# Kernel optimization log

Measured on AMD Instinct MI355X. Metric: run time of the kernel, lower is better.

Reference implementation:

```python
import jax, jax.numpy as jnp
import numpy as np

B, S, P, L, H = 64, 512, 32, 30, 768
FH = 1024  # fc_hidden_size


def setup_inputs() -> dict:
    key = jax.random.key(0)
    ks = jax.random.split(key, 8)
    token_embeddings = jax.random.normal(ks[0], (B, S, H), jnp.float32)
    pooler_output = jax.random.normal(ks[1], (B, H), jnp.float32)
    num_positions = jax.random.randint(ks[2], (B, P), 0, S)
    # labels: 0/1 codes, with trailing slots per example padded with -1 rows
    lab = jax.random.randint(ks[3], (B, P, L), 0, 2).astype(jnp.float32)
    valid = jax.random.randint(ks[4], (B, 1), 8, P + 1)  # num real slots per example
    row = jnp.arange(P)[None, :]
    lab = jnp.where((row < valid)[:, :, None], lab, -1.0)
    num_codes_labels = lab.reshape(B, P * L)
    W1 = jax.random.normal(ks[5], (2 * H, FH), jnp.float32) / np.sqrt(2 * H)
    b1 = jnp.zeros((FH,), jnp.float32)
    W2 = jax.random.normal(ks[6], (FH, FH // 2), jnp.float32) / np.sqrt(FH)
    b2 = jnp.zeros((FH // 2,), jnp.float32)
    W3 = jax.random.normal(ks[7], (FH // 2, L), jnp.float32) / np.sqrt(FH // 2)
    b3 = jnp.zeros((L,), jnp.float32)
    return {"token_embeddings": token_embeddings, "pooler_output": pooler_output,
            "num_positions": num_positions, "num_codes_labels": num_codes_labels,
            "W1": W1, "b1": b1, "W2": W2, "b2": b2, "W3": W3, "b3": b3}


def reference(token_embeddings, pooler_output, num_positions, num_codes_labels,
              W1, b1, W2, b2, W3, b3):
    # gather number-token hidden states: [B, P, H]
    p_hidden = jnp.take_along_axis(token_embeddings, num_positions[:, :, None], axis=1)
    feat = jnp.concatenate(
        [p_hidden, jnp.broadcast_to(pooler_output[:, None, :], p_hidden.shape)], axis=-1)
    # Batch_Net_CLS head. NOTE: original uses nn.LeakyReLU(True) -> negative_slope=1.0,
    # which is mathematically the identity, so the activations are omitted (faithful).
    h = feat @ W1 + b1
    h = h @ W2 + b2
    logits = h @ W3 + b3  # [B, P, L]

    labels = num_codes_labels.reshape(B, -1, L)
    pad_pre = jnp.any(labels != -1.0, axis=-1)  # [B, P] True for real slots
    mf = pad_pre.astype(jnp.float32)

    # BCEWithLogitsLoss over non-pad elements: softplus(x) - x*y, mean
    bce_elem = jax.nn.softplus(logits) - logits * labels
    bce_loss = jnp.sum(bce_elem * mf[:, :, None]) / (jnp.sum(mf) * L)

    binary = (jax.nn.sigmoid(logits) > 0.5).astype(jnp.float32)
    count_out = jnp.sum(binary, axis=-1)
    count_lab = jnp.sum(labels, axis=-1)
    count_loss = jnp.mean((count_out - count_lab) ** 2 * mf)

    # position loss: only slots where both counts are exactly 1 (single-hot)
    eq = (count_out == 1.0) & (count_lab == 1.0)
    pos_out = jnp.argmax(binary, axis=-1).astype(jnp.float32)
    pos_lab = jnp.argmax(labels, axis=-1).astype(jnp.float32)
    n_eq = jnp.sum(eq.astype(jnp.float32))
    pos_sum = jnp.sum((pos_out - pos_lab) ** 2 * eq.astype(jnp.float32))
    position_loss = jnp.where(n_eq > 0, pos_sum / jnp.maximum(n_eq, 1.0), 0.0)

    return bce_loss + 10.0 * count_loss + 5.0 * position_loss
```

## Files before the change

kernel.cpp:

```cpp
#include <hip/hip_runtime.h>
#include <cstddef>
#include <cstdint>

#define Mq   2048
#define Lq   30
#define N1q  1024
#define N2q  512
#define K1q  1536
#define Hq   768
#define NBLK 512
#define Z1   2
#define Z2   4

typedef float    f32x4 __attribute__((ext_vector_type(4)));
typedef _Float16 f16x8 __attribute__((ext_vector_type(8)));

#define GLD16(gptr, lptr) \
  __builtin_amdgcn_global_load_lds((const __attribute__((address_space(1))) void*)(gptr), \
                                   (__attribute__((address_space(3))) void*)(lptr), 16, 0, 0)

__device__ void transpose_tile(const float* __restrict__ src,
                               _Float16* __restrict__ dst,
                               int K, int N, int k0, int n0) {
  __shared__ float T[64][65];
  const int t = threadIdx.x;
  {
    const int kl = t >> 2, nc = (t & 3) * 16;
    const float* s = src + (size_t)(k0 + kl) * N + n0 + nc;
    float4 v0 = *(const float4*)s;
    float4 v1 = *(const float4*)(s + 4);
    float4 v2 = *(const float4*)(s + 8);
    float4 v3 = *(const float4*)(s + 12);
    T[nc + 0][kl] = v0.x; T[nc + 1][kl] = v0.y; T[nc + 2][kl] = v0.z; T[nc + 3][kl] = v0.w;
    T[nc + 4][kl] = v1.x; T[nc + 5][kl] = v1.y; T[nc + 6][kl] = v1.z; T[nc + 7][kl] = v1.w;
    T[nc + 8][kl] = v2.x; T[nc + 9][kl] = v2.y; T[nc +10][kl] = v2.z; T[nc +11][kl] = v2.w;
    T[nc +12][kl] = v3.x; T[nc +13][kl] = v3.y; T[nc +14][kl] = v3.z; T[nc +15][kl] = v3.w;
  }
  __syncthreads();
  {
    const int nl = t >> 2, kc = (t & 3) * 16;
    __align__(16) _Float16 tmp[16];
    #pragma unroll
    for (int i = 0; i < 16; ++i) tmp[i] = (_Float16)T[nl][kc + i];
    _Float16* d = dst + (size_t)(n0 + nl) * K + k0 + kc;
    *(uint4*)d       = *(const uint4*)tmp;
    *(uint4*)(d + 8) = *(const uint4*)(tmp + 8);
  }
}

__global__ __launch_bounds__(256)
void prep_all(const float* __restrict__ tok, const float* __restrict__ pool,
              const int* __restrict__ npos, const float* __restrict__ W1,
              const float* __restrict__ W2, _Float16* __restrict__ A1,
              _Float16* __restrict__ W1T, _Float16* __restrict__ W2T) {
  const int bid = blockIdx.x, tid = threadIdx.x;
  if (bid < 256) {
    const int q = tid >> 5, l32 = tid & 31;
    const int m = bid * 8 + q;
    const int bI = m >> 5, p = m & 31;
    const int pos = npos[bI * 32 + p];
    const float* src1 = tok + ((size_t)bI * 512 + pos) * Hq;
    const float* src2 = pool + (size_t)bI * Hq;
    _Float16* dst = A1 + (size_t)m * K1q;
    for (int g = l32; g < 384; g += 32) {
      const float* s = (g < 192) ? (src1 + g * 4) : (src2 + (g - 192) * 4);
      float4 v = *(const float4*)s;
      __align__(8) _Float16 o[4] = {(_Float16)v.x, (_Float16)v.y, (_Float16)v.z, (_Float16)v.w};
      *(uint2*)(dst + g * 4) = *(const uint2*)o;
    }
  } else if (bid < 640) {
    const int idx = bid - 256;
    transpose_tile(W1, W1T, K1q, N1q, (idx / 16) * 64, (idx % 16) * 64);
  } else {
    const int idx = bid - 640;
    transpose_tile(W2, W2T, N1q, N2q, (idx / 8) * 64, (idx % 8) * 64);
  }
}

__global__ __launch_bounds__(256)
void gemm1_f16(const _Float16* __restrict__ A, const _Float16* __restrict__ BT,
               _Float16* __restrict__ Cpart) {
  __shared__ _Float16 As[128 * 32];
  __shared__ _Float16 Bs[128 * 32];
  const int tid = threadIdx.x, w = tid >> 6, lane = tid & 63;
  const int n0 = blockIdx.x * 128, m0 = blockIdx.y * 128, z = blockIdx.z;
  const int ml = lane & 15, g4 = lane >> 4;
  const int wm = (w >> 1) * 64, wn = (w & 1) * 64;

  f32x4 acc[4][4];
  #pragma unroll
  for (int i = 0; i < 4; ++i)
    #pragma unroll
    for (int j = 0; j < 4; ++j)
      #pragma unroll
      for (int r = 0; r < 4; ++r) acc[i][j][r] = 0.f;

  const int rs0 = w * 32 + (lane >> 2);
  const int cl  = lane & 3;

  for (int it = 0; it < (K1q / Z1) / 32; ++it) {
    const int kt = z * (K1q / Z1) + it * 32;
    __syncthreads();
    #pragma unroll
    for (int t = 0; t < 2; ++t) {
      const int r  = rs0 + t * 16;
      const int cs = cl ^ ((r >> 1) & 3);
      GLD16(A  + (size_t)(m0 + r) * K1q + kt + cs * 8, As + (w * 32 + t * 16) * 32);
      GLD16(BT + (size_t)(n0 + r) * K1q + kt + cs * 8, Bs + (w * 32 + t * 16) * 32);
    }
    __syncthreads();
    f16x8 af[4], bf[4];
    #pragma unroll
    for (int i = 0; i < 4; ++i) {
      const int ar = wm + i * 16 + ml;
      af[i] = *(const f16x8*)(As + ar * 32 + ((g4 ^ ((ar >> 1) & 3)) << 3));
      const int br = wn + i * 16 + ml;
      bf[i] = *(const f16x8*)(Bs + br * 32 + ((g4 ^ ((br >> 1) & 3)) << 3));
    }
    #pragma unroll
    for (int i = 0; i < 4; ++i)
      #pragma unroll
      for (int j = 0; j < 4; ++j)
        acc[i][j] = __builtin_amdgcn_mfma_f32_16x16x32_f16(bf[j], af[i], acc[i][j], 0, 0, 0);
  }

  _Float16* Cp = Cpart + (size_t)z * Mq * N1q;
  #pragma unroll
  for (int i = 0; i < 4; ++i) {
    const int row = m0 + wm + i * 16 + ml;
    #pragma unroll
    for (int j = 0; j < 4; ++j) {
      const int col = n0 + wn + j * 16 + g4 * 4;
      __align__(8) _Float16 o[4] = {(_Float16)acc[i][j][0], (_Float16)acc[i][j][1],
                                    (_Float16)acc[i][j][2], (_Float16)acc[i][j][3]};
      *(uint2*)(Cp + (size_t)row * N1q + col) = *(const uint2*)o;
    }
  }
}

__global__ __launch_bounds__(256)
void gemm2_fused(const _Float16* __restrict__ C1, const float* __restrict__ b1,
                 const _Float16* __restrict__ BT, float* __restrict__ Cpart) {
  __shared__ _Float16 As[128 * 32];
  __shared__ _Float16 Bs[128 * 32];
  const int tid = threadIdx.x, w = tid >> 6, lane = tid & 63;
  const int n0 = blockIdx.x * 128, m0 = blockIdx.y * 128, z = blockIdx.z;
  const int ml = lane & 15, g4 = lane >> 4;
  const int wm = (w >> 1) * 64, wn = (w & 1) * 64;
  const size_t MN1 = (size_t)Mq * N1q;

  f32x4 acc[4][4];
  #pragma unroll
  for (int i = 0; i < 4; ++i)
    #pragma unroll
    for (int j = 0; j < 4; ++j)
      #pragma unroll
      for (int r = 0; r < 4; ++r) acc[i][j][r] = 0.f;

  const int rs0 = w * 32 + (lane >> 2);
  const int cl  = lane & 3;
  const int r2  = tid >> 1, half = tid & 1;

  for (int it = 0; it < (N1q / Z2) / 32; ++it) {
    const int kt = z * (N1q / Z2) + it * 32;
    __syncthreads();
    #pragma unroll
    for (int t = 0; t < 2; ++t) {
      const int r  = rs0 + t * 16;
      const int cs = cl ^ ((r >> 1) & 3);
      GLD16(BT + (size_t)(n0 + r) * N1q + kt + cs * 8, Bs + (w * 32 + t * 16) * 32);
    }
    {
      const _Float16* p = C1 + (size_t)(m0 + r2) * N1q + kt + half * 16;
      f16x8 u0 = *(const f16x8*)p;
      f16x8 u1 = *(const f16x8*)(p + 8);
      f16x8 v0 = *(const f16x8*)(p + MN1);
      f16x8 v1 = *(const f16x8*)(p + MN1 + 8);
      const float* bb = b1 + kt + half * 16;
      f16x8 o0, o1;
      #pragma unroll
      for (int e = 0; e < 8; ++e) {
        o0[e] = (_Float16)((float)u0[e] + (float)v0[e] + bb[e]);
        o1[e] = (_Float16)((float)u1[e] + (float)v1[e] + bb[e + 8]);
      }
      const int s  = (r2 >> 1) & 3;
      *(f16x8*)(As + r2 * 32 + (((half * 2)     ^ s) << 3)) = o0;
      *(f16x8*)(As + r2 * 32 + (((half * 2 + 1) ^ s) << 3)) = o1;
    }
    __syncthreads();
    f16x8 af[4], bf[4];
    #pragma unroll
    for (int i = 0; i < 4; ++i) {
      const int ar = wm + i * 16 + ml;
      af[i] = *(const f16x8*)(As + ar * 32 + ((g4 ^ ((ar >> 1) & 3)) << 3));
      const int br = wn + i * 16 + ml;
      bf[i] = *(const f16x8*)(Bs + br * 32 + ((g4 ^ ((br >> 1) & 3)) << 3));
    }
    #pragma unroll
    for (int i = 0; i < 4; ++i)
      #pragma unroll
      for (int j = 0; j < 4; ++j)
        acc[i][j] = __builtin_amdgcn_mfma_f32_16x16x32_f16(bf[j], af[i], acc[i][j], 0, 0, 0);
  }

  float* Cp = Cpart + (size_t)z * Mq * N2q;
  #pragma unroll
  for (int i = 0; i < 4; ++i) {
    const int row = m0 + wm + i * 16 + ml;
    #pragma unroll
    for (int j = 0; j < 4; ++j) {
      const int col = n0 + wn + j * 16 + g4 * 4;
      *(float4*)(Cp + (size_t)row * N2q + col) = *(const float4*)&acc[i][j];
    }
  }
}

__global__ __launch_bounds__(256)
void loss_kernel(const float* __restrict__ C2, const float* __restrict__ b2,
                 const float* __restrict__ W3, const float* __restrict__ b3,
                 const float* __restrict__ labels, float* __restrict__ part) {
  __shared__ float hrow[4][512];
  __shared__ float red[4][5];
  const int tid = threadIdx.x, w = tid >> 6, lane = tid & 63;
  const int m = blockIdx.x * 4 + w;
  const size_t MN2 = (size_t)Mq * N2q;

  {
    const int k = lane * 8;
    float4 s0 = *(const float4*)(b2 + k);
    float4 s1 = *(const float4*)(b2 + k + 4);
    const float* cp = C2 + (size_t)m * N2q + k;
    #pragma unroll
    for (int z = 0; z < Z2; ++z) {
      float4 v0 = *(const float4*)(cp + (size_t)z * MN2);
      float4 v1 = *(const float4*)(cp + (size_t)z * MN2 + 4);
      s0.x += v0.x; s0.y += v0.y; s0.z += v0.z; s0.w += v0.w;
      s1.x += v1.x; s1.y += v1.y; s1.z += v1.z; s1.w += v1.w;
    }
    *(float4*)&hrow[w][k]     = s0;
    *(float4*)&hrow[w][k + 4] = s1;
  }
  __syncthreads();

  const int c  = lane & 31;
  const int kh = lane >> 5;
  float a0 = 0.f, a1 = 0.f, a2 = 0.f, a3 = 0.f;
  if (c < Lq) {
    const float* hp = hrow[w] + kh * 256;
    const float* wp = W3 + (size_t)(kh * 256) * Lq + c;
    #pragma unroll 4
    for (int i = 0; i < 256; i += 4) {
      a0 = fmaf(hp[i],     wp[(i)     * Lq], a0);
      a1 = fmaf(hp[i + 1], wp[(i + 1) * Lq], a1);
      a2 = fmaf(hp[i + 2], wp[(i + 2) * Lq], a2);
      a3 = fmaf(hp[i + 3], wp[(i + 3) * Lq], a3);
    }
  }
  float a = (a0 + a1) + (a2 + a3);
  a += __shfl_xor(a, 32);

  const bool act = lane < Lq;
  float logit = 0.f, lab = 0.f;
  if (act) {
    logit = a + b3[lane];
    lab = labels[(size_t)m * Lq + lane];
  }

  const unsigned long long validmask = __ballot(act && lab != -1.0f);
  const unsigned long long outmask   = __ballot(act && logit > 0.0f);
  const unsigned long long labmask   = __ballot(act && lab == 1.0f);
  const bool valid = (validmask != 0ULL);
  const int count_out = __popcll(outmask);
  const int count_lab = __popcll(labmask);

  float bce = 0.f;
  if (act && valid) {
    const float x = logit;
    bce = fmaxf(x, 0.f) + log1pf(expf(-fabsf(x))) - x * lab;
  }
  bce += __shfl_xor(bce, 16); bce += __shfl_xor(bce, 8);
  bce += __shfl_xor(bce, 4);  bce += __shfl_xor(bce, 2);
  bce += __shfl_xor(bce, 1);

  if (lane == 0) {
    float pb = 0.f, pv = 0.f, pc = 0.f, pe = 0.f, pp = 0.f;
    if (valid) {
      pb = bce; pv = 1.f;
      const float d = (float)count_out - (float)count_lab;
      pc = d * d;
    }
    if (count_out == 1 && count_lab == 1) {
      const float po = (float)(__ffsll((long long)outmask) - 1);
      const float pl = (float)(__ffsll((long long)labmask) - 1);
      pe = 1.f;
      const float dp = po - pl;
      pp = dp * dp;
    }
    red[w][0] = pb; red[w][1] = pv; red[w][2] = pc; red[w][3] = pe; red[w][4] = pp;
  }
  __syncthreads();
  if (tid < 5) {
    part[blockIdx.x * 5 + tid] =
        red[0][tid] + red[1][tid] + red[2][tid] + red[3][tid];
  }
}

__global__ __launch_bounds__(256)
void finalize_kernel(const float* __restrict__ part, float* __restrict__ out) {
  __shared__ float red[32][5];
  const int t = threadIdx.x;
  if (t < 160) {
    const int j = t % 5, grp = t / 5;
    float s = 0.f;
    for (int i = grp; i < NBLK; i += 32) s += part[i * 5 + j];
    red[grp][j] = s;
  }
  __syncthreads();
  if (t == 0) {
    float t0 = 0.f, t1 = 0.f, t2 = 0.f, t3 = 0.f, t4 = 0.f;
    #pragma unroll
    for (int g = 0; g < 32; ++g) {
      t0 += red[g][0]; t1 += red[g][1]; t2 += red[g][2];
      t3 += red[g][3]; t4 += red[g][4];
    }
    const float bce = t0 / (t1 * (float)Lq);
    const float cnt = 10.0f * t2 / (float)Mq;
    const float pos = (t3 > 0.f) ? 5.0f * t4 / fmaxf(t3, 1.0f) : 0.f;
    out[0] = bce + cnt + pos;
  }
}

extern "C" void kernel_launch(void* const* d_in, const int* in_sizes, int n_in,
                              void* d_out, int out_size, void* d_ws, size_t ws_size,
                              hipStream_t stream) {
  const float* tok    = (const float*)d_in[0];
  const float* pool   = (const float*)d_in[1];
  const int*   npos   = (const int*)  d_in[2];
  const float* labels = (const float*)d_in[3];
  const float* W1     = (const float*)d_in[4];
  const float* b1     = (const float*)d_in[5];
  const float* W2     = (const float*)d_in[6];
  const float* b2     = (const float*)d_in[7];
  const float* W3     = (const float*)d_in[8];
  const float* b3     = (const float*)d_in[9];
  float* out = (float*)d_out;

  char* ws = (char*)d_ws;
  _Float16* A1   = (_Float16*)(ws + 0x00000000);
  _Float16* C1p  = (_Float16*)(ws + 0x00600000);
  _Float16* W1T  = (_Float16*)(ws + 0x00E00000);
  _Float16* W2T  = (_Float16*)(ws + 0x01100000);
  float*    C2p  = (float*)   (ws + 0x01200000);
  float*    part = (float*)   (ws + 0x02200000);

  prep_all<<<768, 256, 0, stream>>>(tok, pool, npos, W1, W2, A1, W1T, W2T);
  gemm1_f16<<<dim3(8, 16, Z1), 256, 0, stream>>>(A1, W1T, C1p);
  gemm2_fused<<<dim3(4, 16, Z2), 256, 0, stream>>>(C1p, b1, W2T, C2p);
  loss_kernel<<<NBLK, 256, 0, stream>>>(C2p, b2, W3, b3, labels, part);
  finalize_kernel<<<1, 256, 0, stream>>>(part, out);
}
```

Before: 203.5 us.

## Fuse all stages into one cooperative persistent kernel with double-buffered GEMMs

Replaces the five separate launches with a single cooperative kernel of 256 blocks that uses grid.sync between the prep, GEMM1, GEMM2, loss and finalize stages. Both GEMM main loops now double-buffer their LDS tiles so the next tile's loads overlap the current MFMAs. The b1 bias is folded algebraically into a precomputed b2' = b2 + b1·W2, which removes the per-element bias add from GEMM2. The aim is to cut launch gaps and load latency. In exchange, grid-wide barriers are added and only 256 blocks run, below the 512 and 768 blocks some stages used before.

```diff
diff --git a/kernel.cpp b/kernel.cpp
--- a/kernel.cpp
+++ b/kernel.cpp
@@ -1,6 +1,9 @@
 #include <hip/hip_runtime.h>
+#include <hip/hip_cooperative_groups.h>
 #include <cstddef>
 #include <cstdint>
+
+namespace cg = cooperative_groups;
 
 #define Mq   2048
 #define Lq   30
@@ -21,8 +24,8 @@
 
 __device__ void transpose_tile(const float* __restrict__ src,
                                _Float16* __restrict__ dst,
-                               int K, int N, int k0, int n0) {
-  __shared__ float T[64][65];
+                               int K, int N, int k0, int n0,
+                               float (*T)[65]) {
   const int t = threadIdx.x;
   {
     const int kl = t >> 2, nc = (t & 3) * 16;
@@ -46,287 +49,335 @@
     *(uint4*)d       = *(const uint4*)tmp;
     *(uint4*)(d + 8) = *(const uint4*)(tmp + 8);
   }
+  __syncthreads();
 }
 
 __global__ __launch_bounds__(256)
-void prep_all(const float* __restrict__ tok, const float* __restrict__ pool,
-              const int* __restrict__ npos, const float* __restrict__ W1,
-              const float* __restrict__ W2, _Float16* __restrict__ A1,
-              _Float16* __restrict__ W1T, _Float16* __restrict__ W2T) {
+void mega(const float* __restrict__ tok, const float* __restrict__ pool,
+          const int* __restrict__ npos, const float* __restrict__ labels,
+          const float* __restrict__ W1, const float* __restrict__ b1,
+          const float* __restrict__ W2, const float* __restrict__ b2,
+          const float* __restrict__ W3, const float* __restrict__ b3,
+          char* __restrict__ ws, float* __restrict__ out)
+{
+  __shared__ __align__(16) unsigned char SMEM[32768];
+
+  _Float16* A1   = (_Float16*)(ws + 0x00000000);
+  _Float16* C1p  = (_Float16*)(ws + 0x00600000);
+  _Float16* W1T  = (_Float16*)(ws + 0x00E00000);
+  _Float16* W2T  = (_Float16*)(ws + 0x01100000);
+  float*    C2p  = (float*)   (ws + 0x01200000);
+  float*    part = (float*)   (ws + 0x02200000);
+  float*    b2p  = (float*)   (ws + 0x02210000);
+
   const int bid = blockIdx.x, tid = threadIdx.x;
-  if (bid < 256) {
-    const int q = tid >> 5, l32 = tid & 31;
-    const int m = bid * 8 + q;
-    const int bI = m >> 5, p = m & 31;
-    const int pos = npos[bI * 32 + p];
-    const float* src1 = tok + ((size_t)bI * 512 + pos) * Hq;
-    const float* src2 = pool + (size_t)bI * Hq;
-    _Float16* dst = A1 + (size_t)m * K1q;
-    for (int g = l32; g < 384; g += 32) {
-      const float* s = (g < 192) ? (src1 + g * 4) : (src2 + (g - 192) * 4);
-      float4 v = *(const float4*)s;
-      __align__(8) _Float16 o[4] = {(_Float16)v.x, (_Float16)v.y, (_Float16)v.z, (_Float16)v.w};
-      *(uint2*)(dst + g * 4) = *(const uint2*)o;
-    }
-  } else if (bid < 640) {
-    const int idx = bid - 256;
-    transpose_tile(W1, W1T, K1q, N1q, (idx / 16) * 64, (idx % 16) * 64);
-  } else {
-    const int idx = bid - 640;
-    transpose_tile(W2, W2T, N1q, N2q, (idx / 8) * 64, (idx % 8) * 64);
-  }
-}
-
-__global__ __launch_bounds__(256)
-void gemm1_f16(const _Float16* __restrict__ A, const _Float16* __restrict__ BT,
-               _Float16* __restrict__ Cpart) {
-  __shared__ _Float16 As[128 * 32];
-  __shared__ _Float16 Bs[128 * 32];
-  const int tid = threadIdx.x, w = tid >> 6, lane = tid & 63;
-  const int n0 = blockIdx.x * 128, m0 = blockIdx.y * 128, z = blockIdx.z;
-  const int ml = lane & 15, g4 = lane >> 4;
-  const int wm = (w >> 1) * 64, wn = (w & 1) * 64;
-
-  f32x4 acc[4][4];
-  #pragma unroll
-  for (int i = 0; i < 4; ++i)
+  const int w = tid >> 6, lane = tid & 63;
+  cg::grid_group grid = cg::this_grid();
+
+  {
+    float (*T)[65] = (float(*)[65])SMEM;
+    #pragma unroll 1
+    for (int i = 0; i < 3; ++i) {
+      const int u = bid + 256 * i;
+      if (u < 256) {
+        const int q = tid >> 5, l32 = tid & 31;
+        const int m = u * 8 + q;
+        const int bI = m >> 5, p = m & 31;
+        const int pos = npos[bI * 32 + p];
+        const float* src1 = tok + ((size_t)bI * 512 + pos) * Hq;
+        const float* src2 = pool + (size_t)bI * Hq;
+        _Float16* dst = A1 + (size_t)m * K1q;
+        for (int g = l32; g < 384; g += 32) {
+          const float* s = (g < 192) ? (src1 + g * 4) : (src2 + (g - 192) * 4);
+          float4 v = *(const float4*)s;
+          __align__(8) _Float16 o[4] = {(_Float16)v.x, (_Float16)v.y, (_Float16)v.z, (_Float16)v.w};
+          *(uint2*)(dst + g * 4) = *(const uint2*)o;
+        }
+      } else if (u < 640) {
+        const int idx = u - 256;
+        transpose_tile(W1, W1T, K1q, N1q, (idx / 16) * 64, (idx % 16) * 64, T);
+      } else {
+        const int idx = u - 640;
+        transpose_tile(W2, W2T, N1q, N2q, (idx / 8) * 64, (idx % 8) * 64, T);
+      }
+    }
+    if (bid < 8) {
+      const int c  = bid * 64 + (tid >> 2);
+      const int ks = (tid & 3) * 256;
+      float s = 0.f;
+      for (int k = 0; k < 256; ++k)
+        s = fmaf(b1[ks + k], W2[(size_t)(ks + k) * N2q + c], s);
+      s += __shfl_xor(s, 1);
+      s += __shfl_xor(s, 2);
+      if ((tid & 3) == 0) b2p[c] = b2[c] + s;
+    }
+  }
+  grid.sync();
+
+  {
+    _Float16* As = (_Float16*)SMEM;
+    _Float16* Bs = (_Float16*)(SMEM + 16384);
+    const int bx = bid & 7, by = (bid >> 3) & 15, z = bid >> 7;
+    const int n0 = bx * 128, m0 = by * 128;
+    const int ml = lane & 15, g4 = lane >> 4;
+    const int wm = (w >> 1) * 64, wn = (w & 1) * 64;
+    const int rs0 = w * 32 + (lane >> 2);
+    const int cl  = lane & 3;
+    const int kbase = z * (K1q / Z1);
+
+    f32x4 acc[4][4];
     #pragma unroll
-    for (int j = 0; j < 4; ++j)
-      #pragma unroll
-      for (int r = 0; r < 4; ++r) acc[i][j][r] = 0.f;
-
-  const int rs0 = w * 32 + (lane >> 2);
-  const int cl  = lane & 3;
-
-  for (int it = 0; it < (K1q / Z1) / 32; ++it) {
-    const int kt = z * (K1q / Z1) + it * 32;
+    for (int i = 0; i < 4; ++i)
+      #pragma unroll
+      for (int j = 0; j < 4; ++j)
+        #pragma unroll
+        for (int r = 0; r < 4; ++r) acc[i][j][r] = 0.f;
+
+    auto stage1 = [&](int it, int b) {
+      const int kt = kbase + it * 32;
+      #pragma unroll
+      for (int t = 0; t < 2; ++t) {
+        const int r  = rs0 + t * 16;
+        const int cs = cl ^ ((r >> 1) & 3);
+        GLD16(A1  + (size_t)(m0 + r) * K1q + kt + cs * 8, As + b * 4096 + (w * 32 + t * 16) * 32);
+        GLD16(W1T + (size_t)(n0 + r) * K1q + kt + cs * 8, Bs + b * 4096 + (w * 32 + t * 16) * 32);
+      }
+    };
+
+    stage1(0, 0);
     __syncthreads();
-    #pragma unroll
-    for (int t = 0; t < 2; ++t) {
-      const int r  = rs0 + t * 16;
-      const int cs = cl ^ ((r >> 1) & 3);
-      GLD16(A  + (size_t)(m0 + r) * K1q + kt + cs * 8, As + (w * 32 + t * 16) * 32);
-      GLD16(BT + (size_t)(n0 + r) * K1q + kt + cs * 8, Bs + (w * 32 + t * 16) * 32);
-    }
-    __syncthreads();
-    f16x8 af[4], bf[4];
+    int cur = 0;
+    #pragma unroll 1
+    for (int it = 0; it < (K1q / Z1) / 32; ++it) {
+      if (it < (K1q / Z1) / 32 - 1) stage1(it + 1, cur ^ 1);
+      f16x8 af[4], bf[4];
+      #pragma unroll
+      for (int i = 0; i < 4; ++i) {
+        const int ar = wm + i * 16 + ml;
+        af[i] = *(const f16x8*)(As + cur * 4096 + ar * 32 + ((g4 ^ ((ar >> 1) & 3)) << 3));
+        const int br = wn + i * 16 + ml;
+        bf[i] = *(const f16x8*)(Bs + cur * 4096 + br * 32 + ((g4 ^ ((br >> 1) & 3)) << 3));
+      }
+      #pragma unroll
+      for (int i = 0; i < 4; ++i)
+        #pragma unroll
+        for (int j = 0; j < 4; ++j)
+          acc[i][j] = __builtin_amdgcn_mfma_f32_16x16x32_f16(bf[j], af[i], acc[i][j], 0, 0, 0);
+      __syncthreads();
+      cur ^= 1;
+    }
+
+    _Float16* Cp = C1p + (size_t)z * Mq * N1q;
     #pragma unroll
     for (int i = 0; i < 4; ++i) {
-      const int ar = wm + i * 16 + ml;
-      af[i] = *(const f16x8*)(As + ar * 32 + ((g4 ^ ((ar >> 1) & 3)) << 3));
-      const int br = wn + i * 16 + ml;
-      bf[i] = *(const f16x8*)(Bs + br * 32 + ((g4 ^ ((br >> 1) & 3)) << 3));
-    }
+      const int row = m0 + wm + i * 16 + ml;
+      #pragma unroll
+      for (int j = 0; j < 4; ++j) {
+        const int col = n0 + wn + j * 16 + g4 * 4;
+        __align__(8) _Float16 o[4] = {(_Float16)acc[i][j][0], (_Float16)acc[i][j][1],
+                                      (_Float16)acc[i][j][2], (_Float16)acc[i][j][3]};
+        *(uint2*)(Cp + (size_t)row * N1q + col) = *(const uint2*)o;
+      }
+    }
+  }
+  grid.sync();
+
+  {
+    _Float16* As = (_Float16*)SMEM;
+    _Float16* Bs = (_Float16*)(SMEM + 16384);
+    const int bx = bid & 3, by = (bid >> 2) & 15, z = bid >> 6;
+    const int n0 = bx * 128, m0 = by * 128;
+    const int ml = lane & 15, g4 = lane >> 4;
+    const int wm = (w >> 1) * 64, wn = (w & 1) * 64;
+    const int rs0 = w * 32 + (lane >> 2);
+    const int cl  = lane & 3;
+    const int r2  = tid >> 1, half = tid & 1;
+    const size_t MN1 = (size_t)Mq * N1q;
+    const int kb2 = z * (N1q / Z2);
+
+    f32x4 acc[4][4];
     #pragma unroll
     for (int i = 0; i < 4; ++i)
       #pragma unroll
       for (int j = 0; j < 4; ++j)
-        acc[i][j] = __builtin_amdgcn_mfma_f32_16x16x32_f16(bf[j], af[i], acc[i][j], 0, 0, 0);
-  }
-
-  _Float16* Cp = Cpart + (size_t)z * Mq * N1q;
-  #pragma unroll
-  for (int i = 0; i < 4; ++i) {
-    const int row = m0 + wm + i * 16 + ml;
-    #pragma unroll
-    for (int j = 0; j < 4; ++j) {
-      const int col = n0 + wn + j * 16 + g4 * 4;
-      __align__(8) _Float16 o[4] = {(_Float16)acc[i][j][0], (_Float16)acc[i][j][1],
-                                    (_Float16)acc[i][j][2], (_Float16)acc[i][j][3]};
-      *(uint2*)(Cp + (size_t)row * N1q + col) = *(const uint2*)o;
-    }
-  }
-}
-
-__global__ __launch_bounds__(256)
-void gemm2_fused(const _Float16* __restrict__ C1, const float* __restrict__ b1,
-                 const _Float16* __restrict__ BT, float* __restrict__ Cpart) {
-  __shared__ _Float16 As[128 * 32];
-  __shared__ _Float16 Bs[128 * 32];
-  const int tid = threadIdx.x, w = tid >> 6, lane = tid & 63;
-  const int n0 = blockIdx.x * 128, m0 = blockIdx.y * 128, z = blockIdx.z;
-  const int ml = lane & 15, g4 = lane >> 4;
-  const int wm = (w >> 1) * 64, wn = (w & 1) * 64;
-  const size_t MN1 = (size_t)Mq * N1q;
-
-  f32x4 acc[4][4];
-  #pragma unroll
-  for (int i = 0; i < 4; ++i)
-    #pragma unroll
-    for (int j = 0; j < 4; ++j)
-      #pragma unroll
-      for (int r = 0; r < 4; ++r) acc[i][j][r] = 0.f;
-
-  const int rs0 = w * 32 + (lane >> 2);
-  const int cl  = lane & 3;
-  const int r2  = tid >> 1, half = tid & 1;
-
-  for (int it = 0; it < (N1q / Z2) / 32; ++it) {
-    const int kt = z * (N1q / Z2) + it * 32;
+        #pragma unroll
+        for (int r = 0; r < 4; ++r) acc[i][j][r] = 0.f;
+
+    f16x8 u0, u1, v0, v1;
+    auto issueA2 = [&](int it) {
+      const _Float16* p = C1p + (size_t)(m0 + r2) * N1q + kb2 + it * 32 + half * 16;
+      u0 = *(const f16x8*)p;         u1 = *(const f16x8*)(p + 8);
+      v0 = *(const f16x8*)(p + MN1); v1 = *(const f16x8*)(p + MN1 + 8);
+    };
+    auto stageB2 = [&](int it, int b) {
+      const int kt = kb2 + it * 32;
+      #pragma unroll
+      for (int t = 0; t < 2; ++t) {
+        const int r  = rs0 + t * 16;
+        const int cs = cl ^ ((r >> 1) & 3);
+        GLD16(W2T + (size_t)(n0 + r) * N1q + kt + cs * 8, Bs + b * 4096 + (w * 32 + t * 16) * 32);
+      }
+    };
+    auto writeA2 = [&](int b) {
+      f16x8 o0, o1;
+      #pragma unroll
+      for (int e = 0; e < 8; ++e) {
+        o0[e] = (_Float16)((float)u0[e] + (float)v0[e]);
+        o1[e] = (_Float16)((float)u1[e] + (float)v1[e]);
+      }
+      const int s = (r2 >> 1) & 3;
+      *(f16x8*)(As + b * 4096 + r2 * 32 + (((half * 2)     ^ s) << 3)) = o0;
+      *(f16x8*)(As + b * 4096 + r2 * 32 + (((half * 2 + 1) ^ s) << 3)) = o1;
+    };
+
+    issueA2(0); stageB2(0, 0); writeA2(0);
     __syncthreads();
-    #pragma unroll
-    for (int t = 0; t < 2; ++t) {
-      const int r  = rs0 + t * 16;
-      const int cs = cl ^ ((r >> 1) & 3);
-      GLD16(BT + (size_t)(n0 + r) * N1q + kt + cs * 8, Bs + (w * 32 + t * 16) * 32);
-    }
-    {
-      const _Float16* p = C1 + (size_t)(m0 + r2) * N1q + kt + half * 16;
-      f16x8 u0 = *(const f16x8*)p;
-      f16x8 u1 = *(const f16x8*)(p + 8);
-      f16x8 v0 = *(const f16x8*)(p + MN1);
-      f16x8 v1 = *(const f16x8*)(p + MN1 + 8);
-      const float* bb = b1 + kt + half * 16;
-      f16x8 o0, o1;
-      #pragma unroll
-      for (int e = 0; e < 8; ++e) {
-        o0[e] = (_Float16)((float)u0[e] + (float)v0[e] + bb[e]);
-        o1[e] = (_Float16)((float)u1[e] + (float)v1[e] + bb[e + 8]);
-      }
-      const int s  = (r2 >> 1) & 3;
-      *(f16x8*)(As + r2 * 32 + (((half * 2)     ^ s) << 3)) = o0;
-      *(f16x8*)(As + r2 * 32 + (((half * 2 + 1) ^ s) << 3)) = o1;
-    }
-    __syncthreads();
-    f16x8 af[4], bf[4];
+    int cur = 0;
+    #pragma unroll 1
+    for (int it = 0; it < (N1q / Z2) / 32; ++it) {
+      if (it < (N1q / Z2) / 32 - 1) { issueA2(it + 1); stageB2(it + 1, cur ^ 1); }
+      f16x8 af[4], bf[4];
+      #pragma unroll
+      for (int i = 0; i < 4; ++i) {
+        const int ar = wm + i * 16 + ml;
+        af[i] = *(const f16x8*)(As + cur * 4096 + ar * 32 + ((g4 ^ ((ar >> 1) & 3)) << 3));
+        const int br = wn + i * 16 + ml;
+        bf[i] = *(const f16x8*)(Bs + cur * 4096 + br * 32 + ((g4 ^ ((br >> 1) & 3)) << 3));
+      }
+      #pragma unroll
+      for (int i = 0; i < 4; ++i)
+        #pragma unroll
+        for (int j = 0; j < 4; ++j)
+          acc[i][j] = __builtin_amdgcn_mfma_f32_16x16x32_f16(bf[j], af[i], acc[i][j], 0, 0, 0);
+      if (it < (N1q / Z2) / 32 - 1) writeA2(cur ^ 1);
+      __syncthreads();
+      cur ^= 1;
+    }
+
+    float* Cp = C2p + (size_t)z * Mq * N2q;
     #pragma unroll
     for (int i = 0; i < 4; ++i) {
-      const int ar = wm + i * 16 + ml;
-      af[i] = *(const f16x8*)(As + ar * 32 + ((g4 ^ ((ar >> 1) & 3)) << 3));
-      const int br = wn + i * 16 + ml;
-      bf[i] = *(const f16x8*)(Bs + br * 32 + ((g4 ^ ((br >> 1) & 3)) << 3));
-    }
-    #pragma unroll
-    for (int i = 0; i < 4; ++i)
-      #pragma unroll
-      for (int j = 0; j < 4; ++j)
-        acc[i][j] = __builtin_amdgcn_mfma_f32_16x16x32_f16(bf[j], af[i], acc[i][j], 0, 0, 0);
-  }
-
-  float* Cp = Cpart + (size_t)z * Mq * N2q;
-  #pragma unroll
-  for (int i = 0; i < 4; ++i) {
-    const int row = m0 + wm + i * 16 + ml;
-    #pragma unroll
-    for (int j = 0; j < 4; ++j) {
-      const int col = n0 + wn + j * 16 + g4 * 4;
-      *(float4*)(Cp + (size_t)row * N2q + col) = *(const float4*)&acc[i][j];
-    }
-  }
-}
-
-__global__ __launch_bounds__(256)
-void loss_kernel(const float* __restrict__ C2, const float* __restrict__ b2,
-                 const float* __restrict__ W3, const float* __restrict__ b3,
-                 const float* __restrict__ labels, float* __restrict__ part) {
-  __shared__ float hrow[4][512];
-  __shared__ float red[4][5];
-  const int tid = threadIdx.x, w = tid >> 6, lane = tid & 63;
-  const int m = blockIdx.x * 4 + w;
-  const size_t MN2 = (size_t)Mq * N2q;
-
-  {
-    const int k = lane * 8;
-    float4 s0 = *(const float4*)(b2 + k);
-    float4 s1 = *(const float4*)(b2 + k + 4);
-    const float* cp = C2 + (size_t)m * N2q + k;
-    #pragma unroll
-    for (int z = 0; z < Z2; ++z) {
-      float4 v0 = *(const float4*)(cp + (size_t)z * MN2);
-      float4 v1 = *(const float4*)(cp + (size_t)z * MN2 + 4);
-      s0.x += v0.x; s0.y += v0.y; s0.z += v0.z; s0.w += v0.w;
-      s1.x += v1.x; s1.y += v1.y; s1.z += v1.z; s1.w += v1.w;
-    }
-    *(float4*)&hrow[w][k]     = s0;
-    *(float4*)&hrow[w][k + 4] = s1;
-  }
-  __syncthreads();
-
-  const int c  = lane & 31;
-  const int kh = lane >> 5;
-  float a0 = 0.f, a1 = 0.f, a2 = 0.f, a3 = 0.f;
-  if (c < Lq) {
-    const float* hp = hrow[w] + kh * 256;
-    const float* wp = W3 + (size_t)(kh * 256) * Lq + c;
-    #pragma unroll 4
-    for (int i = 0; i < 256; i += 4) {
-      a0 = fmaf(hp[i],     wp[(i)     * Lq], a0);
-      a1 = fmaf(hp[i + 1], wp[(i + 1) * Lq], a1);
-      a2 = fmaf(hp[i + 2], wp[(i + 2) * Lq], a2);
-      a3 = fmaf(hp[i + 3], wp[(i + 3) * Lq], a3);
-    }
-  }
-  float a = (a0 + a1) + (a2 + a3);
-  a += __shfl_xor(a, 32);
-
-  const bool act = lane < Lq;
-  float logit = 0.f, lab = 0.f;
-  if (act) {
-    logit = a + b3[lane];
-    lab = labels[(size_t)m * Lq + lane];
-  }
-
-  const unsigned long long validmask = __ballot(act && lab != -1.0f);
-  const unsigned long long outmask   = __ballot(act && logit > 0.0f);
-  const unsigned long long labmask   = __ballot(act && lab == 1.0f);
-  const bool valid = (validmask != 0ULL);
-  const int count_out = __popcll(outmask);
-  const int count_lab = __popcll(labmask);
-
-  float bce = 0.f;
-  if (act && valid) {
-    const float x = logit;
-    bce = fmaxf(x, 0.f) + log1pf(expf(-fabsf(x))) - x * lab;
-  }
-  bce += __shfl_xor(bce, 16); bce += __shfl_xor(bce, 8);
-  bce += __shfl_xor(bce, 4);  bce += __shfl_xor(bce, 2);
-  bce += __shfl_xor(bce, 1);
-
-  if (lane == 0) {
-    float pb = 0.f, pv = 0.f, pc = 0.f, pe = 0.f, pp = 0.f;
-    if (valid) {
-      pb = bce; pv = 1.f;
-      const float d = (float)count_out - (float)count_lab;
-      pc = d * d;
-    }
-    if (count_out == 1 && count_lab == 1) {
-      const float po = (float)(__ffsll((long long)outmask) - 1);
-      const float pl = (float)(__ffsll((long long)labmask) - 1);
-      pe = 1.f;
-      const float dp = po - pl;
-      pp = dp * dp;
-    }
-    red[w][0] = pb; red[w][1] = pv; red[w][2] = pc; red[w][3] = pe; red[w][4] = pp;
-  }
-  __syncthreads();
-  if (tid < 5) {
-    part[blockIdx.x * 5 + tid] =
-        red[0][tid] + red[1][tid] + red[2][tid] + red[3][tid];
-  }
-}
-
-__global__ __launch_bounds__(256)
-void finalize_kernel(const float* __restrict__ part, float* __restrict__ out) {
-  __shared__ float red[32][5];
-  const int t = threadIdx.x;
-  if (t < 160) {
-    const int j = t % 5, grp = t / 5;
-    float s = 0.f;
-    for (int i = grp; i < NBLK; i += 32) s += part[i * 5 + j];
-    red[grp][j] = s;
-  }
-  __syncthreads();
-  if (t == 0) {
-    float t0 = 0.f, t1 = 0.f, t2 = 0.f, t3 = 0.f, t4 = 0.f;
-    #pragma unroll
-    for (int g = 0; g < 32; ++g) {
-      t0 += red[g][0]; t1 += red[g][1]; t2 += red[g][2];
-      t3 += red[g][3]; t4 += red[g][4];
-    }
-    const float bce = t0 / (t1 * (float)Lq);
-    const float cnt = 10.0f * t2 / (float)Mq;
-    const float pos = (t3 > 0.f) ? 5.0f * t4 / fmaxf(t3, 1.0f) : 0.f;
-    out[0] = bce + cnt + pos;
+      const int row = m0 + wm + i * 16 + ml;
+      #pragma unroll
+      for (int j = 0; j < 4; ++j) {
+        const int col = n0 + wn + j * 16 + g4 * 4;
+        *(float4*)(Cp + (size_t)row * N2q + col) = *(const float4*)&acc[i][j];
+      }
+    }
+  }
+  grid.sync();
+
+  {
+    float (*hrow)[512] = (float(*)[512])SMEM;
+    float (*red)[5]    = (float(*)[5])(SMEM + 8192);
+    const size_t MN2 = (size_t)Mq * N2q;
+    #pragma unroll 1
+    for (int i = 0; i < 2; ++i) {
+      const int u = bid * 2 + i;
+      const int m = u * 4 + w;
+      __syncthreads();
+      {
+        const int k = lane * 8;
+        float4 s0 = *(const float4*)(b2p + k);
+        float4 s1 = *(const float4*)(b2p + k + 4);
+        const float* cp = C2p + (size_t)m * N2q + k;
+        #pragma unroll
+        for (int zz = 0; zz < Z2; ++zz) {
+          float4 q0 = *(const float4*)(cp + (size_t)zz * MN2);
+          float4 q1 = *(const float4*)(cp + (size_t)zz * MN2 + 4);
+          s0.x += q0.x; s0.y += q0.y; s0.z += q0.z; s0.w += q0.w;
+          s1.x += q1.x; s1.y += q1.y; s1.z += q1.z; s1.w += q1.w;
+        }
+        *(float4*)&hrow[w][k]     = s0;
+        *(float4*)&hrow[w][k + 4] = s1;
+      }
+      __syncthreads();
+
+      const int c  = lane & 31;
+      const int kh = lane >> 5;
+      float a0 = 0.f, a1 = 0.f, a2 = 0.f, a3 = 0.f;
+      if (c < Lq) {
+        const float* hp = hrow[w] + kh * 256;
+        const float* wp = W3 + (size_t)(kh * 256) * Lq + c;
+        #pragma unroll 4
+        for (int k = 0; k < 256; k += 4) {
+          a0 = fmaf(hp[k],     wp[(k)     * Lq], a0);
+          a1 = fmaf(hp[k + 1], wp[(k + 1) * Lq], a1);
+          a2 = fmaf(hp[k + 2], wp[(k + 2) * Lq], a2);
+          a3 = fmaf(hp[k + 3], wp[(k + 3) * Lq], a3);
+        }
+      }
+      float a = (a0 + a1) + (a2 + a3);
+      a += __shfl_xor(a, 32);
+
+      const bool act = lane < Lq;
+      float logit = 0.f, lab = 0.f;
+      if (act) {
+        logit = a + b3[lane];
+        lab = labels[(size_t)m * Lq + lane];
+      }
+
+      const unsigned long long validmask = __ballot(act && lab != -1.0f);
+      const unsigned long long outmask   = __ballot(act && logit > 0.0f);
+      const unsigned long long labmask   = __ballot(act && lab == 1.0f);
+      const bool valid = (validmask != 0ULL);
+      const int count_out = __popcll(outmask);
+      const int count_lab = __popcll(labmask);
+
+      float bce = 0.f;
+      if (act && valid) {
+        const float x = logit;
+        bce = fmaxf(x, 0.f) + log1pf(expf(-fabsf(x))) - x * lab;
+      }
+      bce += __shfl_xor(bce, 16); bce += __shfl_xor(bce, 8);
+      bce += __shfl_xor(bce, 4);  bce += __shfl_xor(bce, 2);
+      bce += __shfl_xor(bce, 1);
+
+      if (lane == 0) {
+        float pb = 0.f, pv = 0.f, pc = 0.f, pe = 0.f, pp = 0.f;
+        if (valid) {
+          pb = bce; pv = 1.f;
+          const float d = (float)count_out - (float)count_lab;
+          pc = d * d;
+        }
+        if (count_out == 1 && count_lab == 1) {
+          const float po = (float)(__ffsll((long long)outmask) - 1);
+          const float pl = (float)(__ffsll((long long)labmask) - 1);
+          pe = 1.f;
+          const float dp = po - pl;
+          pp = dp * dp;
+        }
+        red[w][0] = pb; red[w][1] = pv; red[w][2] = pc; red[w][3] = pe; red[w][4] = pp;
+      }
+      __syncthreads();
+      if (tid < 5) {
+        part[u * 5 + tid] = red[0][tid] + red[1][tid] + red[2][tid] + red[3][tid];
+      }
+    }
+  }
+  grid.sync();
+
+  if (bid == 0) {
+    float (*fr)[5] = (float(*)[5])SMEM;
+    if (tid < 160) {
+      const int j = tid % 5, grp = tid / 5;
+      float s = 0.f;
+      for (int i = grp; i < NBLK; i += 32) s += part[i * 5 + j];
+      fr[grp][j] = s;
+    }
+    __syncthreads();
+    if (tid == 0) {
+      float t0 = 0.f, t1 = 0.f, t2 = 0.f, t3 = 0.f, t4 = 0.f;
+      #pragma unroll
+      for (int g = 0; g < 32; ++g) {
+        t0 += fr[g][0]; t1 += fr[g][1]; t2 += fr[g][2];
+        t3 += fr[g][3]; t4 += fr[g][4];
+      }
+      const float bce = t0 / (t1 * (float)Lq);
+      const float cnt = 10.0f * t2 / (float)Mq;
+      const float pos = (t3 > 0.f) ? 5.0f * t4 / fmaxf(t3, 1.0f) : 0.f;
+      out[0] = bce + cnt + pos;
+    }
   }
 }
 
@@ -344,18 +395,10 @@
   const float* W3     = (const float*)d_in[8];
   const float* b3     = (const float*)d_in[9];
   float* out = (float*)d_out;
-
-  char* ws = (char*)d_ws;
-  _Float16* A1   = (_Float16*)(ws + 0x00000000);
-  _Float16* C1p  = (_Float16*)(ws + 0x00600000);
-  _Float16* W1T  = (_Float16*)(ws + 0x00E00000);
-  _Float16* W2T  = (_Float16*)(ws + 0x01100000);
-  float*    C2p  = (float*)   (ws + 0x01200000);
-  float*    part = (float*)   (ws + 0x02200000);
-
-  prep_all<<<768, 256, 0, stream>>>(tok, pool, npos, W1, W2, A1, W1T, W2T);
-  gemm1_f16<<<dim3(8, 16, Z1), 256, 0, stream>>>(A1, W1T, C1p);
-  gemm2_fused<<<dim3(4, 16, Z2), 256, 0, stream>>>(C1p, b1, W2T, C2p);
-  loss_kernel<<<NBLK, 256, 0, stream>>>(C2p, b2, W3, b3, labels, part);
-  finalize_kernel<<<1, 256, 0, stream>>>(part, out);
+  char*  ws  = (char*)d_ws;
+
+  void* args[] = { (void*)&tok, (void*)&pool, (void*)&npos, (void*)&labels,
+                   (void*)&W1, (void*)&b1, (void*)&W2, (void*)&b2,
+                   (void*)&W3, (void*)&b3, (void*)&ws, (void*)&out };
+  hipLaunchCooperativeKernel((const void*)mega, dim3(256), dim3(256), args, 0, stream);
 }
```

Result: slower. 358.4 us (+76.1%).

## Replace split-K GEMMs with smaller double-buffered tiles and fused bias epilogues

Applied to the files above, without the earlier changes.

Both GEMMs drop split-K partial buffers in favour of full-K tiles (64x64 for gemm1, 32x64 for gemm2) that use double-buffered LDS staging with BK=64, so the next tile loads while the current one feeds the MFMAs. Bias add moves into each GEMM epilogue. The partial-sum reduction passes in gemm2 and the loss kernel go away, which removes their extra global traffic. In exchange the smaller tiles reuse each loaded element less, and the grids become much larger.

```diff
diff --git a/kernel.cpp b/kernel.cpp
--- a/kernel.cpp
+++ b/kernel.cpp
@@ -9,8 +9,6 @@
 #define K1q  1536
 #define Hq   768
 #define NBLK 512
-#define Z1   2
-#define Z2   4
 
 typedef float    f32x4 __attribute__((ext_vector_type(4)));
 typedef _Float16 f16x8 __attribute__((ext_vector_type(8)));
@@ -78,167 +76,164 @@
 }
 
 __global__ __launch_bounds__(256)
-void gemm1_f16(const _Float16* __restrict__ A, const _Float16* __restrict__ BT,
-               _Float16* __restrict__ Cpart) {
-  __shared__ _Float16 As[128 * 32];
-  __shared__ _Float16 Bs[128 * 32];
+void gemm1_k(const _Float16* __restrict__ A, const _Float16* __restrict__ BT,
+             const float* __restrict__ b1, _Float16* __restrict__ C1) {
+  __shared__ _Float16 As[2][64 * 64];
+  __shared__ _Float16 Bs[2][64 * 64];
   const int tid = threadIdx.x, w = tid >> 6, lane = tid & 63;
-  const int n0 = blockIdx.x * 128, m0 = blockIdx.y * 128, z = blockIdx.z;
+  const int n0 = blockIdx.x * 64, m0 = blockIdx.y * 64;
   const int ml = lane & 15, g4 = lane >> 4;
-  const int wm = (w >> 1) * 64, wn = (w & 1) * 64;
-
-  f32x4 acc[4][4];
+  const int wm = (w >> 1) * 32, wn = (w & 1) * 32;
+  const int lr = lane >> 3, lc = lane & 7;
+
+  f32x4 acc[2][2];
   #pragma unroll
-  for (int i = 0; i < 4; ++i)
-    #pragma unroll
-    for (int j = 0; j < 4; ++j)
+  for (int i = 0; i < 2; ++i)
+    #pragma unroll
+    for (int j = 0; j < 2; ++j)
       #pragma unroll
       for (int r = 0; r < 4; ++r) acc[i][j][r] = 0.f;
 
-  const int rs0 = w * 32 + (lane >> 2);
-  const int cl  = lane & 3;
-
-  for (int it = 0; it < (K1q / Z1) / 32; ++it) {
-    const int kt = z * (K1q / Z1) + it * 32;
+  auto stage = [&](int it, int b) {
+    const int kt = it * 64;
+    #pragma unroll
+    for (int t = 0; t < 2; ++t) {
+      const int r  = w * 16 + t * 8 + lr;
+      const int cs = lc ^ (r & 7);
+      GLD16(A  + (size_t)(m0 + r) * K1q + kt + cs * 8, &As[b][(w * 16 + t * 8) * 64]);
+      GLD16(BT + (size_t)(n0 + r) * K1q + kt + cs * 8, &Bs[b][(w * 16 + t * 8) * 64]);
+    }
+  };
+
+  stage(0, 0);
+  __syncthreads();
+  #pragma unroll 1
+  for (int it = 0; it < 24; ++it) {
+    const int cur = it & 1;
+    if (it < 23) stage(it + 1, cur ^ 1);
+    f16x8 af[2][2], bf[2][2];
+    #pragma unroll
+    for (int i = 0; i < 2; ++i) {
+      const int ar = wm + i * 16 + ml;
+      const int br = wn + i * 16 + ml;
+      #pragma unroll
+      for (int ks = 0; ks < 2; ++ks) {
+        af[i][ks] = *(const f16x8*)&As[cur][ar * 64 + (((ks * 4 + g4) ^ (ar & 7)) << 3)];
+        bf[i][ks] = *(const f16x8*)&Bs[cur][br * 64 + (((ks * 4 + g4) ^ (br & 7)) << 3)];
+      }
+    }
+    #pragma unroll
+    for (int i = 0; i < 2; ++i)
+      #pragma unroll
+      for (int j = 0; j < 2; ++j)
+        #pragma unroll
+        for (int ks = 0; ks < 2; ++ks)
+          acc[i][j] = __builtin_amdgcn_mfma_f32_16x16x32_f16(bf[j][ks], af[i][ks], acc[i][j], 0, 0, 0);
     __syncthreads();
+  }
+
+  #pragma unroll
+  for (int i = 0; i < 2; ++i) {
+    const int row = m0 + wm + i * 16 + ml;
+    #pragma unroll
+    for (int j = 0; j < 2; ++j) {
+      const int col = n0 + wn + j * 16 + g4 * 4;
+      const float4 bv = *(const float4*)(b1 + col);
+      __align__(8) _Float16 o[4] = {(_Float16)(acc[i][j][0] + bv.x),
+                                    (_Float16)(acc[i][j][1] + bv.y),
+                                    (_Float16)(acc[i][j][2] + bv.z),
+                                    (_Float16)(acc[i][j][3] + bv.w)};
+      *(uint2*)(C1 + (size_t)row * N1q + col) = *(const uint2*)o;
+    }
+  }
+}
+
+__global__ __launch_bounds__(256)
+void gemm2_k(const _Float16* __restrict__ A, const _Float16* __restrict__ BT,
+             const float* __restrict__ b2, float* __restrict__ C2) {
+  __shared__ _Float16 As[2][32 * 64];
+  __shared__ _Float16 Bs[2][64 * 64];
+  const int tid = threadIdx.x, w = tid >> 6, lane = tid & 63;
+  const int n0 = blockIdx.x * 64, m0 = blockIdx.y * 32;
+  const int ml = lane & 15, g4 = lane >> 4;
+  const int wm = (w & 1) * 16, wn = (w >> 1) * 32;
+  const int lr = lane >> 3, lc = lane & 7;
+
+  f32x4 acc[2];
+  #pragma unroll
+  for (int j = 0; j < 2; ++j)
+    #pragma unroll
+    for (int r = 0; r < 4; ++r) acc[j][r] = 0.f;
+
+  auto stage = [&](int it, int b) {
+    const int kt = it * 64;
+    {
+      const int r  = w * 8 + lr;
+      const int cs = lc ^ (r & 7);
+      GLD16(A + (size_t)(m0 + r) * N1q + kt + cs * 8, &As[b][(w * 8) * 64]);
+    }
     #pragma unroll
     for (int t = 0; t < 2; ++t) {
-      const int r  = rs0 + t * 16;
-      const int cs = cl ^ ((r >> 1) & 3);
-      GLD16(A  + (size_t)(m0 + r) * K1q + kt + cs * 8, As + (w * 32 + t * 16) * 32);
-      GLD16(BT + (size_t)(n0 + r) * K1q + kt + cs * 8, Bs + (w * 32 + t * 16) * 32);
-    }
+      const int r  = w * 16 + t * 8 + lr;
+      const int cs = lc ^ (r & 7);
+      GLD16(BT + (size_t)(n0 + r) * N1q + kt + cs * 8, &Bs[b][(w * 16 + t * 8) * 64]);
+    }
+  };
+
+  stage(0, 0);
+  __syncthreads();
+  #pragma unroll 1
+  for (int it = 0; it < 16; ++it) {
+    const int cur = it & 1;
+    if (it < 15) stage(it + 1, cur ^ 1);
+    f16x8 af[2], bf[2][2];
+    {
+      const int ar = wm + ml;
+      #pragma unroll
+      for (int ks = 0; ks < 2; ++ks)
+        af[ks] = *(const f16x8*)&As[cur][ar * 64 + (((ks * 4 + g4) ^ (ar & 7)) << 3)];
+    }
+    #pragma unroll
+    for (int j = 0; j < 2; ++j) {
+      const int br = wn + j * 16 + ml;
+      #pragma unroll
+      for (int ks = 0; ks < 2; ++ks)
+        bf[j][ks] = *(const f16x8*)&Bs[cur][br * 64 + (((ks * 4 + g4) ^ (br & 7)) << 3)];
+    }
+    #pragma unroll
+    for (int j = 0; j < 2; ++j)
+      #pragma unroll
+      for (int ks = 0; ks < 2; ++ks)
+        acc[j] = __builtin_amdgcn_mfma_f32_16x16x32_f16(bf[j][ks], af[ks], acc[j], 0, 0, 0);
     __syncthreads();
-    f16x8 af[4], bf[4];
-    #pragma unroll
-    for (int i = 0; i < 4; ++i) {
-      const int ar = wm + i * 16 + ml;
-      af[i] = *(const f16x8*)(As + ar * 32 + ((g4 ^ ((ar >> 1) & 3)) << 3));
-      const int br = wn + i * 16 + ml;
-      bf[i] = *(const f16x8*)(Bs + br * 32 + ((g4 ^ ((br >> 1) & 3)) << 3));
-    }
-    #pragma unroll
-    for (int i = 0; i < 4; ++i)
-      #pragma unroll
-      for (int j = 0; j < 4; ++j)
-        acc[i][j] = __builtin_amdgcn_mfma_f32_16x16x32_f16(bf[j], af[i], acc[i][j], 0, 0, 0);
-  }
-
-  _Float16* Cp = Cpart + (size_t)z * Mq * N1q;
+  }
+
+  const int row = m0 + wm + ml;
   #pragma unroll
-  for (int i = 0; i < 4; ++i) {
-    const int row = m0 + wm + i * 16 + ml;
-    #pragma unroll
-    for (int j = 0; j < 4; ++j) {
-      const int col = n0 + wn + j * 16 + g4 * 4;
-      __align__(8) _Float16 o[4] = {(_Float16)acc[i][j][0], (_Float16)acc[i][j][1],
-                                    (_Float16)acc[i][j][2], (_Float16)acc[i][j][3]};
-      *(uint2*)(Cp + (size_t)row * N1q + col) = *(const uint2*)o;
-    }
-  }
-}
-
-__global__ __launch_bounds__(256)
-void gemm2_fused(const _Float16* __restrict__ C1, const float* __restrict__ b1,
-                 const _Float16* __restrict__ BT, float* __restrict__ Cpart) {
-  __shared__ _Float16 As[128 * 32];
-  __shared__ _Float16 Bs[128 * 32];
-  const int tid = threadIdx.x, w = tid >> 6, lane = tid & 63;
-  const int n0 = blockIdx.x * 128, m0 = blockIdx.y * 128, z = blockIdx.z;
-  const int ml = lane & 15, g4 = lane >> 4;
-  const int wm = (w >> 1) * 64, wn = (w & 1) * 64;
-  const size_t MN1 = (size_t)Mq * N1q;
-
-  f32x4 acc[4][4];
-  #pragma unroll
-  for (int i = 0; i < 4; ++i)
-    #pragma unroll
-    for (int j = 0; j < 4; ++j)
-      #pragma unroll
-      for (int r = 0; r < 4; ++r) acc[i][j][r] = 0.f;
-
-  const int rs0 = w * 32 + (lane >> 2);
-  const int cl  = lane & 3;
-  const int r2  = tid >> 1, half = tid & 1;
-
-  for (int it = 0; it < (N1q / Z2) / 32; ++it) {
-    const int kt = z * (N1q / Z2) + it * 32;
-    __syncthreads();
-    #pragma unroll
-    for (int t = 0; t < 2; ++t) {
-      const int r  = rs0 + t * 16;
-      const int cs = cl ^ ((r >> 1) & 3);
-      GLD16(BT + (size_t)(n0 + r) * N1q + kt + cs * 8, Bs + (w * 32 + t * 16) * 32);
-    }
-    {
-      const _Float16* p = C1 + (size_t)(m0 + r2) * N1q + kt + half * 16;
-      f16x8 u0 = *(const f16x8*)p;
-      f16x8 u1 = *(const f16x8*)(p + 8);
-      f16x8 v0 = *(const f16x8*)(p + MN1);
-      f16x8 v1 = *(const f16x8*)(p + MN1 + 8);
-      const float* bb = b1 + kt + half * 16;
-      f16x8 o0, o1;
-      #pragma unroll
-      for (int e = 0; e < 8; ++e) {
-        o0[e] = (_Float16)((float)u0[e] + (float)v0[e] + bb[e]);
-        o1[e] = (_Float16)((float)u1[e] + (float)v1[e] + bb[e + 8]);
-      }
-      const int s  = (r2 >> 1) & 3;
-      *(f16x8*)(As + r2 * 32 + (((half * 2)     ^ s) << 3)) = o0;
-      *(f16x8*)(As + r2 * 32 + (((half * 2 + 1) ^ s) << 3)) = o1;
-    }
-    __syncthreads();
-    f16x8 af[4], bf[4];
-    #pragma unroll
-    for (int i = 0; i < 4; ++i) {
-      const int ar = wm + i * 16 + ml;
-      af[i] = *(const f16x8*)(As + ar * 32 + ((g4 ^ ((ar >> 1) & 3)) << 3));
-      const int br = wn + i * 16 + ml;
-      bf[i] = *(const f16x8*)(Bs + br * 32 + ((g4 ^ ((br >> 1) & 3)) << 3));
-    }
-    #pragma unroll
-    for (int i = 0; i < 4; ++i)
-      #pragma unroll
-      for (int j = 0; j < 4; ++j)
-        acc[i][j] = __builtin_amdgcn_mfma_f32_16x16x32_f16(bf[j], af[i], acc[i][j], 0, 0, 0);
-  }
-
-  float* Cp = Cpart + (size_t)z * Mq * N2q;
-  #pragma unroll
-  for (int i = 0; i < 4; ++i) {
-    const int row = m0 + wm + i * 16 + ml;
-    #pragma unroll
-    for (int j = 0; j < 4; ++j) {
-      const int col = n0 + wn + j * 16 + g4 * 4;
-      *(float4*)(Cp + (size_t)row * N2q + col) = *(const float4*)&acc[i][j];
-    }
-  }
-}
-
-__global__ __launch_bounds__(256)
-void loss_kernel(const float* __restrict__ C2, const float* __restrict__ b2,
-                 const float* __restrict__ W3, const float* __restrict__ b3,
-                 const float* __restrict__ labels, float* __restrict__ part) {
+  for (int j = 0; j < 2; ++j) {
+    const int col = n0 + wn + j * 16 + g4 * 4;
+    const float4 bv = *(const float4*)(b2 + col);
+    float4 o;
+    o.x = acc[j][0] + bv.x; o.y = acc[j][1] + bv.y;
+    o.z = acc[j][2] + bv.z; o.w = acc[j][3] + bv.w;
+    *(float4*)(C2 + (size_t)row * N2q + col) = o;
+  }
+}
+
+__global__ __launch_bounds__(256)
+void loss_kernel(const float* __restrict__ C2, const float* __restrict__ W3,
+                 const float* __restrict__ b3, const float* __restrict__ labels,
+                 float* __restrict__ part) {
   __shared__ float hrow[4][512];
   __shared__ float red[4][5];
   const int tid = threadIdx.x, w = tid >> 6, lane = tid & 63;
   const int m = blockIdx.x * 4 + w;
-  const size_t MN2 = (size_t)Mq * N2q;
 
   {
     const int k = lane * 8;
-    float4 s0 = *(const float4*)(b2 + k);
-    float4 s1 = *(const float4*)(b2 + k + 4);
     const float* cp = C2 + (size_t)m * N2q + k;
-    #pragma unroll
-    for (int z = 0; z < Z2; ++z) {
-      float4 v0 = *(const float4*)(cp + (size_t)z * MN2);
-      float4 v1 = *(const float4*)(cp + (size_t)z * MN2 + 4);
-      s0.x += v0.x; s0.y += v0.y; s0.z += v0.z; s0.w += v0.w;
-      s1.x += v1.x; s1.y += v1.y; s1.z += v1.z; s1.w += v1.w;
-    }
-    *(float4*)&hrow[w][k]     = s0;
-    *(float4*)&hrow[w][k + 4] = s1;
+    *(float4*)&hrow[w][k]     = *(const float4*)cp;
+    *(float4*)&hrow[w][k + 4] = *(const float4*)(cp + 4);
   }
   __syncthreads();
 
@@ -347,15 +342,15 @@
 
   char* ws = (char*)d_ws;
   _Float16* A1   = (_Float16*)(ws + 0x00000000);
-  _Float16* C1p  = (_Float16*)(ws + 0x00600000);
-  _Float16* W1T  = (_Float16*)(ws + 0x00E00000);
-  _Float16* W2T  = (_Float16*)(ws + 0x01100000);
-  float*    C2p  = (float*)   (ws + 0x01200000);
-  float*    part = (float*)   (ws + 0x02200000);
+  _Float16* W1T  = (_Float16*)(ws + 0x00600000);
+  _Float16* W2T  = (_Float16*)(ws + 0x00900000);
+  _Float16* C1   = (_Float16*)(ws + 0x00A00000);
+  float*    C2   = (float*)   (ws + 0x00E00000);
+  float*    part = (float*)   (ws + 0x01200000);
 
   prep_all<<<768, 256, 0, stream>>>(tok, pool, npos, W1, W2, A1, W1T, W2T);
-  gemm1_f16<<<dim3(8, 16, Z1), 256, 0, stream>>>(A1, W1T, C1p);
-  gemm2_fused<<<dim3(4, 16, Z2), 256, 0, stream>>>(C1p, b1, W2T, C2p);
-  loss_kernel<<<NBLK, 256, 0, stream>>>(C2p, b2, W3, b3, labels, part);
+  gemm1_k<<<dim3(16, 32), 256, 0, stream>>>(A1, W1T, b1, C1);
+  gemm2_k<<<dim3(8, 64), 256, 0, stream>>>(C1, W2T, b2, C2);
+  loss_kernel<<<NBLK, 256, 0, stream>>>(C2, W3, b3, labels, part);
   finalize_kernel<<<1, 256, 0, stream>>>(part, out);
 }
```

Result: faster. 194.2 us (-4.6%).
